# Kernel optimization log

Measured on AMD Instinct MI355X. Metric: run time of the kernel, lower is better.

Reference implementation:

```python
import jax, jax.numpy as jnp
import numpy as np


def _safe_div(x, y):
    # avoid NaNs in branches that are masked out by jnp.where
    return x / jnp.where(jnp.abs(y) < 1e-12, 1.0, y)


def _closest_point_region(p, a, b, c):
    """Ericson closest-point-on-triangle, vectorized.
    p: [B,n,1,3]; a,b,c: [B,1,m,3] -> (dist2 [B,n,m], region [B,n,m] int32).
    Region codes: 0=vertA 1=vertB 2=vertC 3=edgeAB 4=edgeAC 5=edgeBC 6=face.
    """
    ab = b - a; ac = c - a; cb = c - b
    ap = p - a; bp = p - b; cp = p - c
    d1 = (ab * ap).sum(-1); d2 = (ac * ap).sum(-1)
    d3 = (ab * bp).sum(-1); d4 = (ac * bp).sum(-1)
    d5 = (ab * cp).sum(-1); d6 = (ac * cp).sum(-1)
    vc = d1 * d4 - d3 * d2
    vb = d5 * d2 - d1 * d6
    va = d3 * d6 - d5 * d4

    # candidate closest points per region
    v_ab = jnp.clip(_safe_div(d1, d1 - d3), 0.0, 1.0)
    v_ac = jnp.clip(_safe_div(d2, d2 - d6), 0.0, 1.0)
    v_bc = jnp.clip(_safe_div(d4 - d3, (d4 - d3) + (d5 - d6)), 0.0, 1.0)
    denom = va + vb + vc
    v_f = _safe_div(vb, denom); w_f = _safe_div(vc, denom)

    q_face = a + v_f[..., None] * ab + w_f[..., None] * ac
    q_ab = a + v_ab[..., None] * ab
    q_ac = a + v_ac[..., None] * ac
    q_bc = b + v_bc[..., None] * cb

    # region conditions (Ericson priority: a, b, ab, c, ac, bc, face)
    cond_a = (d1 <= 0) & (d2 <= 0)
    cond_b = (d3 >= 0) & (d4 <= d3)
    cond_ab = (vc <= 0) & (d1 >= 0) & (d3 <= 0)
    cond_c = (d6 >= 0) & (d5 <= d6)
    cond_ac = (vb <= 0) & (d2 >= 0) & (d6 <= 0)
    cond_bc = (va <= 0) & (d4 - d3 >= 0) & (d5 - d6 >= 0)

    def sel(cond, qc, code, q, region):
        q = jnp.where(cond[..., None], qc, q)
        region = jnp.where(cond, code, region)
        return q, region

    # apply lowest priority first so higher-priority regions overwrite
    q = q_face
    region = jnp.full(q.shape[:-1], 6, dtype=jnp.int32)
    q, region = sel(cond_bc, q_bc, 5, q, region)
    q, region = sel(cond_ac, q_ac, 4, q, region)
    q, region = sel(cond_c, c, 2, q, region)
    q, region = sel(cond_ab, q_ab, 3, q, region)
    q, region = sel(cond_b, b, 1, q, region)
    q, region = sel(cond_a, a, 0, q, region)

    diff = p - q
    dist2 = (diff * diff).sum(-1)  # squared distance, as in chamfer-style kernels
    return dist2, region


def setup_inputs() -> dict:
    key = jax.random.key(0)
    k1, k2, k3, k4 = jax.random.split(key, 4)
    B, n, m = 4, 4096, 512
    xyz1 = jax.random.normal(k1, (B, n, 3), dtype=jnp.float32)
    tri1 = jax.random.normal(k2, (B, m, 3), dtype=jnp.float32)
    tri2 = jax.random.normal(k3, (B, m, 3), dtype=jnp.float32)
    tri3 = jax.random.normal(k4, (B, m, 3), dtype=jnp.float32)
    return {"xyz1": xyz1, "tri1": tri1, "tri2": tri2, "tri3": tri3}


def reference(xyz1, tri1, tri2, tri3):
    p = xyz1[:, :, None, :]       # [B,n,1,3]
    a = tri1[:, None, :, :]       # [B,1,m,3]
    b = tri2[:, None, :, :]
    c = tri3[:, None, :, :]
    dist2, region = _closest_point_region(p, a, b, c)  # [B,n,m]
    index = jnp.argmin(dist2, axis=-1).astype(jnp.int32)            # [B,n]
    dist = jnp.min(dist2, axis=-1)                                  # [B,n]
    point = jnp.take_along_axis(region, index[..., None].astype(jnp.int64), axis=-1)[..., 0]
    return dist, point, index
```

## Files before the change

kernel.cpp:

```cpp
#include <hip/hip_runtime.h>
#include <math.h>

#define BB 4
#define NN 4096
#define MM 512
#define PTS 16
#define CHUNKS 32
#define MCHUNK (MM / CHUNKS)
#define TPB (PTS * CHUNKS)

__device__ __forceinline__ float safercp(float y) {
    float yy = (fabsf(y) < 1e-12f) ? 1.0f : y;
    return __builtin_amdgcn_rcpf(yy);
}

__device__ __forceinline__ float clip01(float x) {
    return fminf(fmaxf(x, 0.0f), 1.0f);
}

__global__ __launch_bounds__(TPB) void tridist_kernel(
    const float* __restrict__ xyz1, const float* __restrict__ tri1,
    const float* __restrict__ tri2, const float* __restrict__ tri3,
    float* __restrict__ out)
{
    __shared__ float4 sT[MM * 3 + MM / 16];
    __shared__ float rd[TPB];
    __shared__ int   ri[TPB];
    __shared__ int   rr[TPB];

    const int t   = threadIdx.x;
    const int bpb = NN / PTS;
    const int b   = blockIdx.x / bpb;
    const int pb  = blockIdx.x % bpb;
    const int pt  = t & (PTS - 1);
    const int ch  = t >> 4;
    const int point = pb * PTS + pt;

    {
        const int jj = t;
        const int base = jj * 3 + (jj >> 4);
        const float* g1 = tri1 + ((size_t)b * MM + jj) * 3;
        const float* g2 = tri2 + ((size_t)b * MM + jj) * 3;
        const float* g3 = tri3 + ((size_t)b * MM + jj) * 3;
        sT[base + 0] = make_float4(g1[0], g1[1], g1[2], g2[0]);
        sT[base + 1] = make_float4(g2[1], g2[2], g3[0], g3[1]);
        sT[base + 2] = make_float4(g3[2], 0.0f, 0.0f, 0.0f);
    }
    __syncthreads();

    const int gidx = b * NN + point;
    const float px = xyz1[gidx * 3 + 0];
    const float py = xyz1[gidx * 3 + 1];
    const float pz = xyz1[gidx * 3 + 2];

    float bestd = INFINITY;
    int bestj = 0, bestr = 6;

    for (int i = 0; i < MCHUNK; ++i) {
        const int j = ch * MCHUNK + i;
        const int base = j * 3 + ch;
        const float4 r0 = sT[base + 0];
        const float4 r1 = sT[base + 1];
        const float cz  = sT[base + 2].x;
        const float ax = r0.x, ay = r0.y, az = r0.z;
        const float bx = r0.w, by = r1.x, bz = r1.y;
        const float cx = r1.z, cy = r1.w;

        const float abx = bx-ax, aby = by-ay, abz = bz-az;
        const float acx = cx-ax, acy = cy-ay, acz = cz-az;
        const float cbx = cx-bx, cby = cy-by, cbz = cz-bz;
        const float apx = px-ax, apy = py-ay, apz = pz-az;
        const float bpx = px-bx, bpy = py-by, bpz = pz-bz;
        const float cpx = px-cx, cpy = py-cy, cpz = pz-cz;

        const float d1 = fmaf(abz, apz, fmaf(aby, apy, abx*apx));
        const float d2 = fmaf(acz, apz, fmaf(acy, apy, acx*apx));
        const float d3 = fmaf(abz, bpz, fmaf(aby, bpy, abx*bpx));
        const float d4 = fmaf(acz, bpz, fmaf(acy, bpy, acx*bpx));
        const float d5 = fmaf(abz, cpz, fmaf(aby, cpy, abx*cpx));
        const float d6 = fmaf(acz, cpz, fmaf(acy, cpy, acx*cpx));

        const float vc = fmaf(d1, d4, -(d3*d2));
        const float vb = fmaf(d5, d2, -(d1*d6));
        const float va = fmaf(d3, d6, -(d5*d4));

        const float t43 = d4 - d3;
        const float t56 = d5 - d6;
        const float denom = va + vb + vc;

        const float v_ab = clip01(d1 * safercp(d1 - d3));
        const float v_ac = clip01(d2 * safercp(d2 - d6));
        const float v_bc = clip01(t43 * safercp(t43 + t56));
        const float rden = safercp(denom);
        const float v_f = vb * rden;
        const float w_f = vc * rden;

        float qx = fmaf(w_f, acx, fmaf(v_f, abx, ax));
        float qy = fmaf(w_f, acy, fmaf(v_f, aby, ay));
        float qz = fmaf(w_f, acz, fmaf(v_f, abz, az));
        int reg = 6;

        const bool c_bc = (va <= 0.0f) && (t43 >= 0.0f) && (t56 >= 0.0f);
        if (c_bc) { qx = fmaf(v_bc, cbx, bx); qy = fmaf(v_bc, cby, by); qz = fmaf(v_bc, cbz, bz); reg = 5; }
        const bool c_ac = (vb <= 0.0f) && (d2 >= 0.0f) && (d6 <= 0.0f);
        if (c_ac) { qx = fmaf(v_ac, acx, ax); qy = fmaf(v_ac, acy, ay); qz = fmaf(v_ac, acz, az); reg = 4; }
        const bool c_c = (d6 >= 0.0f) && (d5 <= d6);
        if (c_c) { qx = cx; qy = cy; qz = cz; reg = 2; }
        const bool c_ab = (vc <= 0.0f) && (d1 >= 0.0f) && (d3 <= 0.0f);
        if (c_ab) { qx = fmaf(v_ab, abx, ax); qy = fmaf(v_ab, aby, ay); qz = fmaf(v_ab, abz, az); reg = 3; }
        const bool c_b = (d3 >= 0.0f) && (d4 <= d3);
        if (c_b) { qx = bx; qy = by; qz = bz; reg = 1; }
        const bool c_a = (d1 <= 0.0f) && (d2 <= 0.0f);
        if (c_a) { qx = ax; qy = ay; qz = az; reg = 0; }

        const float dx = px - qx;
        const float dy = py - qy;
        const float dz = pz - qz;
        const float dist2 = fmaf(dz, dz, fmaf(dy, dy, dx*dx));

        if (dist2 < bestd) { bestd = dist2; bestj = j; bestr = reg; }
    }

    rd[t] = bestd; ri[t] = bestj; rr[t] = bestr;
    __syncthreads();

    if (ch == 0) {
        float bd = rd[pt];
        int bi = ri[pt], br = rr[pt];
        for (int k = 1; k < CHUNKS; ++k) {
            const float dk = rd[k * PTS + pt];
            if (dk < bd) { bd = dk; bi = ri[k * PTS + pt]; br = rr[k * PTS + pt]; }
        }
        out[gidx]           = bd;
        out[BB*NN + gidx]   = (float)br;
        out[2*BB*NN + gidx] = (float)bi;
    }
}

extern "C" void kernel_launch(void* const* d_in, const int* in_sizes, int n_in,
                              void* d_out, int out_size, void* d_ws, size_t ws_size,
                              hipStream_t stream) {
    const float* xyz1 = (const float*)d_in[0];
    const float* tri1 = (const float*)d_in[1];
    const float* tri2 = (const float*)d_in[2];
    const float* tri3 = (const float*)d_in[3];
    float* out = (float*)d_out;

    dim3 grid(BB * (NN / PTS));
    dim3 block(TPB);
    tridist_kernel<<<grid, block, 0, stream>>>(xyz1, tri1, tri2, tri3, out);
}
```

Before: 86.40 us.

## Precompute per-triangle invariants in LDS and process two points per thread

Each triangle's edge vectors, dot products with its vertices, and reciprocals of squared edge lengths and the Gram determinant are now computed once per block and stored in LDS. This replaces the per-pair subtractions and the four reciprocals, and it relies on the algebraic identities d1-d3=|ab|^2 and denom=Gram determinant. Each thread now handles two points per triangle load, halving the grid and amortizing LDS reads, and the best region is packed together with the index into a single int. The risk is larger LDS use per block (7 float4 per triangle), which may reduce occupancy, plus more register pressure and slight rounding differences from the reformulated dot products.

After: 79.69 us. 7.8% less time.

```diff
diff --git a/kernel.cpp b/kernel.cpp
--- a/kernel.cpp
+++ b/kernel.cpp
@@ -5,9 +5,10 @@
 #define NN 4096
 #define MM 512
 #define PTS 16
+#define NPT 2
 #define CHUNKS 32
 #define MCHUNK (MM / CHUNKS)
-#define TPB (PTS * CHUNKS)
+#define TPB 512
 
 __device__ __forceinline__ float safercp(float y) {
     float yy = (fabsf(y) < 1e-12f) ? 1.0f : y;
@@ -23,117 +24,149 @@
     const float* __restrict__ tri2, const float* __restrict__ tri3,
     float* __restrict__ out)
 {
-    __shared__ float4 sT[MM * 3 + MM / 16];
-    __shared__ float rd[TPB];
-    __shared__ int   ri[TPB];
-    __shared__ int   rr[TPB];
+    __shared__ float4 sT[MM * 7 + MM / 16];
 
-    const int t   = threadIdx.x;
-    const int bpb = NN / PTS;
-    const int b   = blockIdx.x / bpb;
-    const int pb  = blockIdx.x % bpb;
-    const int pt  = t & (PTS - 1);
-    const int ch  = t >> 4;
-    const int point = pb * PTS + pt;
+    const int t  = threadIdx.x;
+    const int b  = blockIdx.x >> 7;
+    const int pb = blockIdx.x & 127;
+    const int pt = t & (PTS - 1);
+    const int ch = t >> 4;
 
     {
         const int jj = t;
-        const int base = jj * 3 + (jj >> 4);
         const float* g1 = tri1 + ((size_t)b * MM + jj) * 3;
         const float* g2 = tri2 + ((size_t)b * MM + jj) * 3;
         const float* g3 = tri3 + ((size_t)b * MM + jj) * 3;
-        sT[base + 0] = make_float4(g1[0], g1[1], g1[2], g2[0]);
-        sT[base + 1] = make_float4(g2[1], g2[2], g3[0], g3[1]);
-        sT[base + 2] = make_float4(g3[2], 0.0f, 0.0f, 0.0f);
+        const float ax = g1[0], ay = g1[1], az = g1[2];
+        const float bx = g2[0], by = g2[1], bz = g2[2];
+        const float cx = g3[0], cy = g3[1], cz = g3[2];
+        const float abx = bx-ax, aby = by-ay, abz = bz-az;
+        const float acx = cx-ax, acy = cy-ay, acz = cz-az;
+        const float cbx = cx-bx, cby = cy-by, cbz = cz-bz;
+        const float aba  = fmaf(abz, az, fmaf(aby, ay, abx*ax));
+        const float abb  = fmaf(abz, bz, fmaf(aby, by, abx*bx));
+        const float abc_ = fmaf(abz, cz, fmaf(aby, cy, abx*cx));
+        const float aca  = fmaf(acz, az, fmaf(acy, ay, acx*ax));
+        const float acb_ = fmaf(acz, bz, fmaf(acy, by, acx*bx));
+        const float acc_ = fmaf(acz, cz, fmaf(acy, cy, acx*cx));
+        const float ab2  = fmaf(abz, abz, fmaf(aby, aby, abx*abx));
+        const float ac2  = fmaf(acz, acz, fmaf(acy, acy, acx*acx));
+        const float cb2  = fmaf(cbz, cbz, fmaf(cby, cby, cbx*cbx));
+        const float abac = fmaf(abz, acz, fmaf(aby, acy, abx*acx));
+        const float gdet = fmaf(ab2, ac2, -(abac*abac));
+        const int base = jj * 7 + (jj >> 4);
+        sT[base + 0] = make_float4(ax, ay, az, bx);
+        sT[base + 1] = make_float4(by, bz, cx, cy);
+        sT[base + 2] = make_float4(cz, abx, aby, abz);
+        sT[base + 3] = make_float4(acx, acy, acz, cbx);
+        sT[base + 4] = make_float4(cby, cbz, aba, abb);
+        sT[base + 5] = make_float4(abc_, aca, acb_, acc_);
+        sT[base + 6] = make_float4(safercp(ab2), safercp(ac2), safercp(cb2), safercp(gdet));
     }
     __syncthreads();
 
-    const int gidx = b * NN + point;
-    const float px = xyz1[gidx * 3 + 0];
-    const float py = xyz1[gidx * 3 + 1];
-    const float pz = xyz1[gidx * 3 + 2];
+    float px[NPT], py[NPT], pz[NPT];
+#pragma unroll
+    for (int np = 0; np < NPT; ++np) {
+        const int gi = b * NN + pb * 32 + np * PTS + pt;
+        px[np] = xyz1[gi*3 + 0];
+        py[np] = xyz1[gi*3 + 1];
+        pz[np] = xyz1[gi*3 + 2];
+    }
 
-    float bestd = INFINITY;
-    int bestj = 0, bestr = 6;
+    float bestd[NPT] = {INFINITY, INFINITY};
+    int   bestc[NPT] = {0, 0};
 
     for (int i = 0; i < MCHUNK; ++i) {
         const int j = ch * MCHUNK + i;
-        const int base = j * 3 + ch;
+        const int base = j * 7 + ch;
         const float4 r0 = sT[base + 0];
         const float4 r1 = sT[base + 1];
-        const float cz  = sT[base + 2].x;
+        const float4 r2 = sT[base + 2];
+        const float4 r3 = sT[base + 3];
+        const float4 r4 = sT[base + 4];
+        const float4 r5 = sT[base + 5];
+        const float4 r6 = sT[base + 6];
         const float ax = r0.x, ay = r0.y, az = r0.z;
         const float bx = r0.w, by = r1.x, bz = r1.y;
-        const float cx = r1.z, cy = r1.w;
+        const float cx = r1.z, cy = r1.w, cz = r2.x;
+        const float abx = r2.y, aby = r2.z, abz = r2.w;
+        const float acx = r3.x, acy = r3.y, acz = r3.z;
+        const float cbx = r3.w, cby = r4.x, cbz = r4.y;
+        const float aba = r4.z, abb = r4.w;
+        const float abc_ = r5.x, aca = r5.y, acb_ = r5.z, acc_ = r5.w;
+        const float rab2 = r6.x, rac2 = r6.y, rcb2 = r6.z, rden = r6.w;
 
-        const float abx = bx-ax, aby = by-ay, abz = bz-az;
-        const float acx = cx-ax, acy = cy-ay, acz = cz-az;
-        const float cbx = cx-bx, cby = cy-by, cbz = cz-bz;
-        const float apx = px-ax, apy = py-ay, apz = pz-az;
-        const float bpx = px-bx, bpy = py-by, bpz = pz-bz;
-        const float cpx = px-cx, cpy = py-cy, cpz = pz-cz;
+#pragma unroll
+        for (int np = 0; np < NPT; ++np) {
+            const float s1 = fmaf(abz, pz[np], fmaf(aby, py[np], abx*px[np]));
+            const float s2 = fmaf(acz, pz[np], fmaf(acy, py[np], acx*px[np]));
+            const float d1 = s1 - aba, d3 = s1 - abb, d5 = s1 - abc_;
+            const float d2 = s2 - aca, d4 = s2 - acb_, d6 = s2 - acc_;
 
-        const float d1 = fmaf(abz, apz, fmaf(aby, apy, abx*apx));
-        const float d2 = fmaf(acz, apz, fmaf(acy, apy, acx*apx));
-        const float d3 = fmaf(abz, bpz, fmaf(aby, bpy, abx*bpx));
-        const float d4 = fmaf(acz, bpz, fmaf(acy, bpy, acx*bpx));
-        const float d5 = fmaf(abz, cpz, fmaf(aby, cpy, abx*cpx));
-        const float d6 = fmaf(acz, cpz, fmaf(acy, cpy, acx*cpx));
+            const float vc = fmaf(d1, d4, -(d3*d2));
+            const float vb = fmaf(d5, d2, -(d1*d6));
+            const float va = fmaf(d3, d6, -(d5*d4));
 
-        const float vc = fmaf(d1, d4, -(d3*d2));
-        const float vb = fmaf(d5, d2, -(d1*d6));
-        const float va = fmaf(d3, d6, -(d5*d4));
+            const float t43 = d4 - d3;
+            const float t56 = d5 - d6;
 
-        const float t43 = d4 - d3;
-        const float t56 = d5 - d6;
-        const float denom = va + vb + vc;
+            const float v_ab = clip01(d1 * rab2);
+            const float v_ac = clip01(d2 * rac2);
+            const float v_bc = clip01(t43 * rcb2);
+            const float v_f = vb * rden;
+            const float w_f = vc * rden;
 
-        const float v_ab = clip01(d1 * safercp(d1 - d3));
-        const float v_ac = clip01(d2 * safercp(d2 - d6));
-        const float v_bc = clip01(t43 * safercp(t43 + t56));
-        const float rden = safercp(denom);
-        const float v_f = vb * rden;
-        const float w_f = vc * rden;
+            float qx = fmaf(w_f, acx, fmaf(v_f, abx, ax));
+            float qy = fmaf(w_f, acy, fmaf(v_f, aby, ay));
+            float qz = fmaf(w_f, acz, fmaf(v_f, abz, az));
+            int reg = 6;
 
-        float qx = fmaf(w_f, acx, fmaf(v_f, abx, ax));
-        float qy = fmaf(w_f, acy, fmaf(v_f, aby, ay));
-        float qz = fmaf(w_f, acz, fmaf(v_f, abz, az));
-        int reg = 6;
+            const bool c_bc = (va <= 0.0f) && (t43 >= 0.0f) && (t56 >= 0.0f);
+            if (c_bc) { qx = fmaf(v_bc, cbx, bx); qy = fmaf(v_bc, cby, by); qz = fmaf(v_bc, cbz, bz); reg = 5; }
+            const bool c_ac = (vb <= 0.0f) && (d2 >= 0.0f) && (d6 <= 0.0f);
+            if (c_ac) { qx = fmaf(v_ac, acx, ax); qy = fmaf(v_ac, acy, ay); qz = fmaf(v_ac, acz, az); reg = 4; }
+            const bool c_c = (d6 >= 0.0f) && (d5 <= d6);
+            if (c_c) { qx = cx; qy = cy; qz = cz; reg = 2; }
+            const bool c_ab = (vc <= 0.0f) && (d1 >= 0.0f) && (d3 <= 0.0f);
+            if (c_ab) { qx = fmaf(v_ab, abx, ax); qy = fmaf(v_ab, aby, ay); qz = fmaf(v_ab, abz, az); reg = 3; }
+            const bool c_b = (d3 >= 0.0f) && (d4 <= d3);
+            if (c_b) { qx = bx; qy = by; qz = bz; reg = 1; }
+            const bool c_a = (d1 <= 0.0f) && (d2 <= 0.0f);
+            if (c_a) { qx = ax; qy = ay; qz = az; reg = 0; }
 
-        const bool c_bc = (va <= 0.0f) && (t43 >= 0.0f) && (t56 >= 0.0f);
-        if (c_bc) { qx = fmaf(v_bc, cbx, bx); qy = fmaf(v_bc, cby, by); qz = fmaf(v_bc, cbz, bz); reg = 5; }
-        const bool c_ac = (vb <= 0.0f) && (d2 >= 0.0f) && (d6 <= 0.0f);
-        if (c_ac) { qx = fmaf(v_ac, acx, ax); qy = fmaf(v_ac, acy, ay); qz = fmaf(v_ac, acz, az); reg = 4; }
-        const bool c_c = (d6 >= 0.0f) && (d5 <= d6);
-        if (c_c) { qx = cx; qy = cy; qz = cz; reg = 2; }
-        const bool c_ab = (vc <= 0.0f) && (d1 >= 0.0f) && (d3 <= 0.0f);
-        if (c_ab) { qx = fmaf(v_ab, abx, ax); qy = fmaf(v_ab, aby, ay); qz = fmaf(v_ab, abz, az); reg = 3; }
-        const bool c_b = (d3 >= 0.0f) && (d4 <= d3);
-        if (c_b) { qx = bx; qy = by; qz = bz; reg = 1; }
-        const bool c_a = (d1 <= 0.0f) && (d2 <= 0.0f);
-        if (c_a) { qx = ax; qy = ay; qz = az; reg = 0; }
+            const float dx = px[np] - qx;
+            const float dy = py[np] - qy;
+            const float dz = pz[np] - qz;
+            const float dist2 = fmaf(dz, dz, fmaf(dy, dy, dx*dx));
 
-        const float dx = px - qx;
-        const float dy = py - qy;
-        const float dz = pz - qz;
-        const float dist2 = fmaf(dz, dz, fmaf(dy, dy, dx*dx));
-
-        if (dist2 < bestd) { bestd = dist2; bestj = j; bestr = reg; }
+            if (dist2 < bestd[np]) { bestd[np] = dist2; bestc[np] = (j << 3) | reg; }
+        }
     }
 
-    rd[t] = bestd; ri[t] = bestj; rr[t] = bestr;
+    __syncthreads();
+    float* rdu = (float*)sT;
+    int*   rcu = (int*)(rdu + NPT * TPB);
+#pragma unroll
+    for (int np = 0; np < NPT; ++np) {
+        rdu[np * TPB + t] = bestd[np];
+        rcu[np * TPB + t] = bestc[np];
+    }
     __syncthreads();
 
-    if (ch == 0) {
-        float bd = rd[pt];
-        int bi = ri[pt], br = rr[pt];
-        for (int k = 1; k < CHUNKS; ++k) {
-            const float dk = rd[k * PTS + pt];
-            if (dk < bd) { bd = dk; bi = ri[k * PTS + pt]; br = rr[k * PTS + pt]; }
+    if (t < 32) {
+        const int np = t >> 4;
+        const int p  = t & 15;
+        float bd = INFINITY; int bc = 0;
+        for (int k = 0; k < CHUNKS; ++k) {
+            const float dk = rdu[np * TPB + k * PTS + p];
+            const int   ck = rcu[np * TPB + k * PTS + p];
+            if (dk < bd) { bd = dk; bc = ck; }
         }
-        out[gidx]           = bd;
-        out[BB*NN + gidx]   = (float)br;
-        out[2*BB*NN + gidx] = (float)bi;
+        const int gidx = b * NN + pb * 32 + t;
+        out[gidx]             = bd;
+        out[BB*NN + gidx]     = (float)(bc & 7);
+        out[2*BB*NN + gidx]   = (float)(bc >> 3);
     }
 }
 
@@ -146,7 +179,7 @@
     const float* tri3 = (const float*)d_in[3];
     float* out = (float*)d_out;
 
-    dim3 grid(BB * (NN / PTS));
+    dim3 grid(BB * (NN / 32));
     dim3 block(TPB);
     tridist_kernel<<<grid, block, 0, stream>>>(xyz1, tri1, tri2, tri3, out);
 }
```
